# Kernel optimization log

Hardware: AMD Instinct MI355X
Metric: run time of the kernel (lower is better)

Reference implementation:

```python
import jax, jax.numpy as jnp
import numpy as np

DIM = 128
B, N = 2, 72


def setup_inputs() -> dict:
    key = jax.random.key(0)
    ks = jax.random.split(key, 6)
    s = 1.0 / np.sqrt(DIM)
    s3 = 1.0 / np.sqrt(3 * DIM)
    return {
        "node_emb": jax.random.normal(ks[0], (B * N, DIM), dtype=jnp.float32),
        "path_emb": jax.random.normal(ks[1], (B, N, N, DIM), dtype=jnp.float32),
        "W_hz": jax.random.uniform(ks[2], (DIM, DIM), minval=-s, maxval=s, dtype=jnp.float32),
        "b_hz": jax.random.uniform(ks[3], (DIM,), minval=-s, maxval=s, dtype=jnp.float32),
        "W_zz": jax.random.uniform(ks[4], (3 * DIM, DIM), minval=-s3, maxval=s3, dtype=jnp.float32),
        "b_zz": jax.random.uniform(ks[5], (DIM,), minval=-s3, maxval=s3, dtype=jnp.float32),
    }


def reference(node_emb, path_emb, W_hz, b_hz, W_zz, b_zz):
    b, n, _, d = path_emb.shape
    # z = W_hz(path_emb)
    z = jnp.einsum('bijd,de->bije', path_emb, W_hz) + b_hz
    # tropical (max-plus) triangle aggregation: out[b,i,j,d] = max_k z[b,i,k,d] + z[b,k,j,d]
    z_conv = jnp.max(z[:, :, :, None, :] + z[:, None, :, :, :], axis=2)  # (b,n,n,d)
    # path_aggr with mode 'max' -> elementwise max of z_conv and z
    z = jnp.maximum(z_conv, z)
    ne = node_emb.reshape(b, n, d)
    n_i = jnp.broadcast_to(ne[:, :, None, :], (b, n, n, d))
    n_j = jnp.broadcast_to(ne[:, None, :, :], (b, n, n, d))
    zc = jnp.concatenate([n_i, z, n_j], axis=-1)  # (b,n,n,3d)
    out = jax.nn.relu(jnp.einsum('bijc,ce->bije', zc, W_zz) + b_zz)
    return out
```

## Files before the change

kernel.cpp:

```cpp
#include <hip/hip_runtime.h>

#define DIM 128
#define NN 72
#define BB 2
#define NSQ (NN*NN)
#define NROWS (BB*NSQ)
#define BN (BB*NN)
#define ZBLOCKS (NROWS/16)
#define NODEBLK 9

__global__ __launch_bounds__(256, 4) void k_phase1(const float* __restrict__ path,
                                                   const float* __restrict__ Whz,
                                                   const float* __restrict__ bhz,
                                                   float* __restrict__ z,
                                                   float* __restrict__ zT,
                                                   const float* __restrict__ node,
                                                   const float* __restrict__ Wzz,
                                                   float* __restrict__ P1,
                                                   float* __restrict__ P3) {
    __shared__ float rows[16 * DIM];
    const int t = threadIdx.x;

    if (blockIdx.x >= NODEBLK) {
        const int r0 = (blockIdx.x - NODEBLK) * 16;
        {
            float4* rs = (float4*)rows;
            const float4* pg = (const float4*)(path + r0 * DIM);
            rs[t]       = pg[t];
            rs[t + 256] = pg[t + 256];
        }
        __syncthreads();

        const int e2 = t & 63;
        const int rg = t >> 6;
        float2 bz = *(const float2*)&bhz[2 * e2];
        float2 acc[4];
#pragma unroll
        for (int r = 0; r < 4; r++) acc[r] = bz;

        const float* Wp = Whz + 2 * e2;
        float2 w0[4], w1[4], n0[4], n1[4];
#pragma unroll
        for (int dd = 0; dd < 4; dd++) {
            w0[dd] = *(const float2*)&Wp[dd * DIM];
            w1[dd] = *(const float2*)&Wp[(4 + dd) * DIM];
        }
        for (int d8 = 0; d8 < 16; d8++) {
            if (d8 < 15) {
#pragma unroll
                for (int dd = 0; dd < 4; dd++) {
                    n0[dd] = *(const float2*)&Wp[(8 * d8 + 8 + dd) * DIM];
                    n1[dd] = *(const float2*)&Wp[(8 * d8 + 12 + dd) * DIM];
                }
            }
            float4 pa[4], pb[4];
#pragma unroll
            for (int r = 0; r < 4; r++) {
                pa[r] = *(const float4*)&rows[(rg + 4 * r) * DIM + 8 * d8];
                pb[r] = *(const float4*)&rows[(rg + 4 * r) * DIM + 8 * d8 + 4];
            }
#pragma unroll
            for (int dd = 0; dd < 4; dd++)
#pragma unroll
                for (int r = 0; r < 4; r++) {
                    float pv = ((const float*)&pa[r])[dd];
                    acc[r].x = fmaf(pv, w0[dd].x, acc[r].x);
                    acc[r].y = fmaf(pv, w0[dd].y, acc[r].y);
                }
#pragma unroll
            for (int dd = 0; dd < 4; dd++)
#pragma unroll
                for (int r = 0; r < 4; r++) {
                    float pv = ((const float*)&pb[r])[dd];
                    acc[r].x = fmaf(pv, w1[dd].x, acc[r].x);
                    acc[r].y = fmaf(pv, w1[dd].y, acc[r].y);
                }
#pragma unroll
            for (int dd = 0; dd < 4; dd++) { w0[dd] = n0[dd]; w1[dd] = n1[dd]; }
        }
#pragma unroll
        for (int r = 0; r < 4; r++) {
            int row = r0 + rg + 4 * r;
            *(float2*)&z[row * DIM + 2 * e2] = acc[r];
            int b  = row / NSQ;
            int ij = row - b * NSQ;
            int i  = ij / NN;
            int j  = ij - i * NN;
            *(float2*)&zT[(b * NSQ + j * NN + i) * DIM + 2 * e2] = acc[r];
        }
    } else {
        const int r0 = blockIdx.x * 16;
        {
            float4* rs = (float4*)rows;
            const float4* ng = (const float4*)(node + r0 * DIM);
            rs[t]       = ng[t];
            rs[t + 256] = ng[t + 256];
        }
        __syncthreads();

        const int e2 = t & 63;
        const int rg = t >> 6;
        float2 a1[4], a3[4];
#pragma unroll
        for (int r = 0; r < 4; r++) {
            a1[r] = make_float2(0.f, 0.f);
            a3[r] = make_float2(0.f, 0.f);
        }

        const float* W1p = Wzz + 2 * e2;
        const float* W3p = Wzz + 2 * DIM * DIM + 2 * e2;
        float2 u0[4], u1[4], v0[4], v1[4];
        float2 un0[4], un1[4], vn0[4], vn1[4];
#pragma unroll
        for (int dd = 0; dd < 4; dd++) {
            u0[dd] = *(const float2*)&W1p[dd * DIM];
            u1[dd] = *(const float2*)&W1p[(4 + dd) * DIM];
            v0[dd] = *(const float2*)&W3p[dd * DIM];
            v1[dd] = *(const float2*)&W3p[(4 + dd) * DIM];
        }
        for (int d8 = 0; d8 < 16; d8++) {
            if (d8 < 15) {
#pragma unroll
                for (int dd = 0; dd < 4; dd++) {
                    un0[dd] = *(const float2*)&W1p[(8 * d8 + 8 + dd) * DIM];
                    un1[dd] = *(const float2*)&W1p[(8 * d8 + 12 + dd) * DIM];
                    vn0[dd] = *(const float2*)&W3p[(8 * d8 + 8 + dd) * DIM];
                    vn1[dd] = *(const float2*)&W3p[(8 * d8 + 12 + dd) * DIM];
                }
            }
            float4 pa[4], pb[4];
#pragma unroll
            for (int r = 0; r < 4; r++) {
                pa[r] = *(const float4*)&rows[(rg + 4 * r) * DIM + 8 * d8];
                pb[r] = *(const float4*)&rows[(rg + 4 * r) * DIM + 8 * d8 + 4];
            }
#pragma unroll
            for (int dd = 0; dd < 4; dd++)
#pragma unroll
                for (int r = 0; r < 4; r++) {
                    float pv = ((const float*)&pa[r])[dd];
                    a1[r].x = fmaf(pv, u0[dd].x, a1[r].x);
                    a1[r].y = fmaf(pv, u0[dd].y, a1[r].y);
                    a3[r].x = fmaf(pv, v0[dd].x, a3[r].x);
                    a3[r].y = fmaf(pv, v0[dd].y, a3[r].y);
                }
#pragma unroll
            for (int dd = 0; dd < 4; dd++)
#pragma unroll
                for (int r = 0; r < 4; r++) {
                    float pv = ((const float*)&pb[r])[dd];
                    a1[r].x = fmaf(pv, u1[dd].x, a1[r].x);
                    a1[r].y = fmaf(pv, u1[dd].y, a1[r].y);
                    a3[r].x = fmaf(pv, v1[dd].x, a3[r].x);
                    a3[r].y = fmaf(pv, v1[dd].y, a3[r].y);
                }
#pragma unroll
            for (int dd = 0; dd < 4; dd++) {
                u0[dd] = un0[dd]; u1[dd] = un1[dd];
                v0[dd] = vn0[dd]; v1[dd] = vn1[dd];
            }
        }
#pragma unroll
        for (int r = 0; r < 4; r++) {
            int m = r0 + rg + 4 * r;
            *(float2*)&P1[m * DIM + 2 * e2] = a1[r];
            *(float2*)&P3[m * DIM + 2 * e2] = a3[r];
        }
    }
}

__global__ __launch_bounds__(256, 3) void k_trop_out(
        const float* __restrict__ z,   const float* __restrict__ zT,
        const float* __restrict__ Wzz, const float* __restrict__ bzz,
        const float* __restrict__ P1,  const float* __restrict__ P3,
        float* __restrict__ out) {
    __shared__ float rows[16 * DIM];
    __shared__ float comb[16 * DIM];
    const int t   = threadIdx.x;
    const int blk = blockIdx.x;
    const int b   = blk / 324;
    const int rem = blk - b * 324;
    const int it  = rem / 18;
    const int jt  = rem - it * 18;
    const int i0 = it * 4, j0 = jt * 4;
    const int d  = t & 127;
    const int ty = t >> 7;
    const float* zb  = z  + b * NSQ * DIM;
    const float* zTb = zT + b * NSQ * DIM;

    {
        float acc[16];
#pragma unroll
        for (int q = 0; q < 16; q++) acc[q] = -3.402823466e38f;

        float cur[32], nxt[32];
#pragma unroll
        for (int kk = 0; kk < 4; kk++) {
            int k = ty + 2 * kk;
#pragma unroll
            for (int s = 0; s < 4; s++) {
                cur[kk * 8 + s]     = zb [((i0 + s) * NN + k) * DIM + d];
                cur[kk * 8 + 4 + s] = zTb[((j0 + s) * NN + k) * DIM + d];
            }
        }
        for (int g = 0; g < 9; g++) {
            if (g < 8) {
#pragma unroll
                for (int kk = 0; kk < 4; kk++) {
                    int k = ty + 2 * kk + 8 * (g + 1);
#pragma unroll
                    for (int s = 0; s < 4; s++) {
                        nxt[kk * 8 + s]     = zb [((i0 + s) * NN + k) * DIM + d];
                        nxt[kk * 8 + 4 + s] = zTb[((j0 + s) * NN + k) * DIM + d];
                    }
                }
            }
#pragma unroll
            for (int kk = 0; kk < 4; kk++)
#pragma unroll
                for (int a = 0; a < 4; a++)
#pragma unroll
                    for (int c = 0; c < 4; c++)
                        acc[a * 4 + c] = fmaxf(acc[a * 4 + c],
                                               cur[kk * 8 + a] + cur[kk * 8 + 4 + c]);
#pragma unroll
            for (int q = 0; q < 32; q++) cur[q] = nxt[q];
        }

        if (ty == 1) {
#pragma unroll
            for (int q = 0; q < 16; q++) comb[q * DIM + d] = acc[q];
        }
        __syncthreads();
        if (ty == 0) {
#pragma unroll
            for (int a = 0; a < 4; a++)
#pragma unroll
                for (int c = 0; c < 4; c++) {
                    int q = a * 4 + c;
                    float m = fmaxf(acc[q], comb[q * DIM + d]);
                    int idx = ((i0 + a) * NN + (j0 + c)) * DIM + d;
                    rows[q * DIM + d] = fmaxf(m, zb[idx]);
                }
        }
    }
    __syncthreads();

    {
        const int e2 = t & 63;
        const int rg = t >> 6;
        float2 acc[4];
#pragma unroll
        for (int r = 0; r < 4; r++) acc[r] = make_float2(0.f, 0.f);

        const float* Wp = Wzz + DIM * DIM + 2 * e2;
        float2 w0[4], w1[4], n0[4], n1[4];
#pragma unroll
        for (int dd = 0; dd < 4; dd++) {
            w0[dd] = *(const float2*)&Wp[dd * DIM];
            w1[dd] = *(const float2*)&Wp[(4 + dd) * DIM];
        }
        for (int d8 = 0; d8 < 16; d8++) {
            if (d8 < 15) {
#pragma unroll
                for (int dd = 0; dd < 4; dd++) {
                    n0[dd] = *(const float2*)&Wp[(8 * d8 + 8 + dd) * DIM];
                    n1[dd] = *(const float2*)&Wp[(8 * d8 + 12 + dd) * DIM];
                }
            }
            float4 pa[4], pb[4];
#pragma unroll
            for (int r = 0; r < 4; r++) {
                pa[r] = *(const float4*)&rows[(rg + 4 * r) * DIM + 8 * d8];
                pb[r] = *(const float4*)&rows[(rg + 4 * r) * DIM + 8 * d8 + 4];
            }
#pragma unroll
            for (int dd = 0; dd < 4; dd++)
#pragma unroll
                for (int r = 0; r < 4; r++) {
                    float pv = ((const float*)&pa[r])[dd];
                    acc[r].x = fmaf(pv, w0[dd].x, acc[r].x);
                    acc[r].y = fmaf(pv, w0[dd].y, acc[r].y);
                }
#pragma unroll
            for (int dd = 0; dd < 4; dd++)
#pragma unroll
                for (int r = 0; r < 4; r++) {
                    float pv = ((const float*)&pb[r])[dd];
                    acc[r].x = fmaf(pv, w1[dd].x, acc[r].x);
                    acc[r].y = fmaf(pv, w1[dd].y, acc[r].y);
                }
#pragma unroll
            for (int dd = 0; dd < 4; dd++) { w0[dd] = n0[dd]; w1[dd] = n1[dd]; }
        }

        float2 bz = *(const float2*)&bzz[2 * e2];
#pragma unroll
        for (int r = 0; r < 4; r++) {
            int q = rg + 4 * r;
            int a = q >> 2, c = q & 3;
            int orow = b * NSQ + (i0 + a) * NN + (j0 + c);
            float2 v1 = *(const float2*)&P1[(b * NN + i0 + a) * DIM + 2 * e2];
            float2 v3 = *(const float2*)&P3[(b * NN + j0 + c) * DIM + 2 * e2];
            float ox = fmaxf(acc[r].x + v1.x + v3.x + bz.x, 0.f);
            float oy = fmaxf(acc[r].y + v1.y + v3.y + bz.y, 0.f);
            *(float2*)&out[orow * DIM + 2 * e2] = make_float2(ox, oy);
        }
    }
}

extern "C" void kernel_launch(void* const* d_in, const int* in_sizes, int n_in,
                              void* d_out, int out_size, void* d_ws, size_t ws_size,
                              hipStream_t stream) {
    const float* node = (const float*)d_in[0];
    const float* path = (const float*)d_in[1];
    const float* Whz  = (const float*)d_in[2];
    const float* bhz  = (const float*)d_in[3];
    const float* Wzz  = (const float*)d_in[4];
    const float* bzz  = (const float*)d_in[5];
    float* out = (float*)d_out;

    float* z  = (float*)d_ws;
    float* zT = z  + NROWS * DIM;
    float* P1 = zT + NROWS * DIM;
    float* P3 = P1 + BN * DIM;

    hipLaunchKernelGGL(k_phase1,   dim3(ZBLOCKS + NODEBLK), dim3(256), 0, stream,
                       path, Whz, bhz, z, zT, node, Wzz, P1, P3);
    hipLaunchKernelGGL(k_trop_out, dim3(BB * 18 * 18),      dim3(256), 0, stream,
                       z, zT, Wzz, bzz, P1, P3, out);
}
```

Baseline: 110.3 us.

## Halve tropical output tile to 2x4 and double-buffer k-loads without copies

The tropical max-plus kernel now processes a 2x4 (i,j) tile per block instead of 4x4, which doubles the grid to 1296 blocks and halves shared memory and register use so that occupancy can rise to 4 blocks per CU. The software pipeline now ping-pongs between two register buffers instead of copying nxt into cur each step. The output GEMV is restructured so each thread computes one output column for 4 rows with scalar loads. The smaller tile lowers register pressure and improves load balance, but each z column is reused across fewer outputs, so global traffic for z goes up, and the W rows are reloaded by twice as many blocks.

```diff
diff --git a/kernel.cpp b/kernel.cpp
--- a/kernel.cpp
+++ b/kernel.cpp
@@ -169,72 +169,72 @@
     }
 }
 
-__global__ __launch_bounds__(256, 3) void k_trop_out(
+__global__ __launch_bounds__(256, 4) void k_trop_out(
         const float* __restrict__ z,   const float* __restrict__ zT,
         const float* __restrict__ Wzz, const float* __restrict__ bzz,
         const float* __restrict__ P1,  const float* __restrict__ P3,
         float* __restrict__ out) {
-    __shared__ float rows[16 * DIM];
-    __shared__ float comb[16 * DIM];
+    __shared__ float rows[8 * DIM];
+    __shared__ float comb[8 * DIM];
     const int t   = threadIdx.x;
     const int blk = blockIdx.x;
-    const int b   = blk / 324;
-    const int rem = blk - b * 324;
+    const int b   = blk / 648;
+    const int rem = blk - b * 648;
     const int it  = rem / 18;
     const int jt  = rem - it * 18;
-    const int i0 = it * 4, j0 = jt * 4;
+    const int i0 = it * 2, j0 = jt * 4;
     const int d  = t & 127;
     const int ty = t >> 7;
     const float* zb  = z  + b * NSQ * DIM;
     const float* zTb = zT + b * NSQ * DIM;
 
     {
-        float acc[16];
-#pragma unroll
-        for (int q = 0; q < 16; q++) acc[q] = -3.402823466e38f;
-
-        float cur[32], nxt[32];
-#pragma unroll
-        for (int kk = 0; kk < 4; kk++) {
-            int k = ty + 2 * kk;
-#pragma unroll
-            for (int s = 0; s < 4; s++) {
-                cur[kk * 8 + s]     = zb [((i0 + s) * NN + k) * DIM + d];
-                cur[kk * 8 + 4 + s] = zTb[((j0 + s) * NN + k) * DIM + d];
-            }
-        }
-        for (int g = 0; g < 9; g++) {
-            if (g < 8) {
-#pragma unroll
-                for (int kk = 0; kk < 4; kk++) {
-                    int k = ty + 2 * kk + 8 * (g + 1);
-#pragma unroll
-                    for (int s = 0; s < 4; s++) {
-                        nxt[kk * 8 + s]     = zb [((i0 + s) * NN + k) * DIM + d];
-                        nxt[kk * 8 + 4 + s] = zTb[((j0 + s) * NN + k) * DIM + d];
-                    }
-                }
-            }
+        float acc[8];
+#pragma unroll
+        for (int q = 0; q < 8; q++) acc[q] = -3.402823466e38f;
+
+        float A[24], B[24];
+
+        auto loadg = [&](float* buf, int g) {
+#pragma unroll
+            for (int kk = 0; kk < 4; kk++) {
+                int k = ty + 2 * kk + 8 * g;
+#pragma unroll
+                for (int s = 0; s < 2; s++)
+                    buf[kk * 6 + s] = zb[((i0 + s) * NN + k) * DIM + d];
+#pragma unroll
+                for (int s = 0; s < 4; s++)
+                    buf[kk * 6 + 2 + s] = zTb[((j0 + s) * NN + k) * DIM + d];
+            }
+        };
+        auto compg = [&](const float* buf) {
 #pragma unroll
             for (int kk = 0; kk < 4; kk++)
 #pragma unroll
-                for (int a = 0; a < 4; a++)
+                for (int a = 0; a < 2; a++)
 #pragma unroll
                     for (int c = 0; c < 4; c++)
                         acc[a * 4 + c] = fmaxf(acc[a * 4 + c],
-                                               cur[kk * 8 + a] + cur[kk * 8 + 4 + c]);
-#pragma unroll
-            for (int q = 0; q < 32; q++) cur[q] = nxt[q];
-        }
+                                               buf[kk * 6 + a] + buf[kk * 6 + 2 + c]);
+        };
+
+        loadg(A, 0);
+        for (int g = 0; g < 8; g += 2) {
+            loadg(B, g + 1);
+            compg(A);
+            loadg(A, g + 2);
+            compg(B);
+        }
+        compg(A);
 
         if (ty == 1) {
 #pragma unroll
-            for (int q = 0; q < 16; q++) comb[q * DIM + d] = acc[q];
+            for (int q = 0; q < 8; q++) comb[q * DIM + d] = acc[q];
         }
         __syncthreads();
         if (ty == 0) {
 #pragma unroll
-            for (int a = 0; a < 4; a++)
+            for (int a = 0; a < 2; a++)
 #pragma unroll
                 for (int c = 0; c < 4; c++) {
                     int q = a * 4 + c;
@@ -247,64 +247,38 @@
     __syncthreads();
 
     {
-        const int e2 = t & 63;
-        const int rg = t >> 6;
-        float2 acc[4];
-#pragma unroll
-        for (int r = 0; r < 4; r++) acc[r] = make_float2(0.f, 0.f);
-
-        const float* Wp = Wzz + DIM * DIM + 2 * e2;
-        float2 w0[4], w1[4], n0[4], n1[4];
-#pragma unroll
-        for (int dd = 0; dd < 4; dd++) {
-            w0[dd] = *(const float2*)&Wp[dd * DIM];
-            w1[dd] = *(const float2*)&Wp[(4 + dd) * DIM];
-        }
+        const int e  = t & 127;
+        const int rr = t >> 7;
+        float a4[4] = {0.f, 0.f, 0.f, 0.f};
+
+        const float* Wp = Wzz + DIM * DIM + e;
+        float w[8], wn[8];
+#pragma unroll
+        for (int dd = 0; dd < 8; dd++) w[dd] = Wp[dd * DIM];
         for (int d8 = 0; d8 < 16; d8++) {
             if (d8 < 15) {
 #pragma unroll
-                for (int dd = 0; dd < 4; dd++) {
-                    n0[dd] = *(const float2*)&Wp[(8 * d8 + 8 + dd) * DIM];
-                    n1[dd] = *(const float2*)&Wp[(8 * d8 + 12 + dd) * DIM];
-                }
-            }
-            float4 pa[4], pb[4];
-#pragma unroll
-            for (int r = 0; r < 4; r++) {
-                pa[r] = *(const float4*)&rows[(rg + 4 * r) * DIM + 8 * d8];
-                pb[r] = *(const float4*)&rows[(rg + 4 * r) * DIM + 8 * d8 + 4];
-            }
-#pragma unroll
-            for (int dd = 0; dd < 4; dd++)
-#pragma unroll
-                for (int r = 0; r < 4; r++) {
-                    float pv = ((const float*)&pa[r])[dd];
-                    acc[r].x = fmaf(pv, w0[dd].x, acc[r].x);
-                    acc[r].y = fmaf(pv, w0[dd].y, acc[r].y);
-                }
-#pragma unroll
-            for (int dd = 0; dd < 4; dd++)
-#pragma unroll
-                for (int r = 0; r < 4; r++) {
-                    float pv = ((const float*)&pb[r])[dd];
-                    acc[r].x = fmaf(pv, w1[dd].x, acc[r].x);
-                    acc[r].y = fmaf(pv, w1[dd].y, acc[r].y);
-                }
-#pragma unroll
-            for (int dd = 0; dd < 4; dd++) { w0[dd] = n0[dd]; w1[dd] = n1[dd]; }
-        }
-
-        float2 bz = *(const float2*)&bzz[2 * e2];
-#pragma unroll
-        for (int r = 0; r < 4; r++) {
-            int q = rg + 4 * r;
+                for (int dd = 0; dd < 8; dd++)
+                    wn[dd] = Wp[(8 * d8 + 8 + dd) * DIM];
+            }
+#pragma unroll
+            for (int dd = 0; dd < 8; dd++)
+#pragma unroll
+                for (int s = 0; s < 4; s++)
+                    a4[s] = fmaf(rows[(rr * 4 + s) * DIM + 8 * d8 + dd], w[dd], a4[s]);
+#pragma unroll
+            for (int dd = 0; dd < 8; dd++) w[dd] = wn[dd];
+        }
+
+        float bz = bzz[e];
+#pragma unroll
+        for (int s = 0; s < 4; s++) {
+            int q = rr * 4 + s;
             int a = q >> 2, c = q & 3;
             int orow = b * NSQ + (i0 + a) * NN + (j0 + c);
-            float2 v1 = *(const float2*)&P1[(b * NN + i0 + a) * DIM + 2 * e2];
-            float2 v3 = *(const float2*)&P3[(b * NN + j0 + c) * DIM + 2 * e2];
-            float ox = fmaxf(acc[r].x + v1.x + v3.x + bz.x, 0.f);
-            float oy = fmaxf(acc[r].y + v1.y + v3.y + bz.y, 0.f);
-            *(float2*)&out[orow * DIM + 2 * e2] = make_float2(ox, oy);
+            float v1 = P1[(b * NN + i0 + a) * DIM + e];
+            float v3 = P3[(b * NN + j0 + c) * DIM + e];
+            out[orow * DIM + e] = fmaxf(a4[s] + v1 + v3 + bz, 0.f);
         }
     }
 }
@@ -327,6 +301,6 @@
 
     hipLaunchKernelGGL(k_phase1,   dim3(ZBLOCKS + NODEBLK), dim3(256), 0, stream,
                        path, Whz, bhz, z, zT, node, Wzz, P1, P3);
-    hipLaunchKernelGGL(k_trop_out, dim3(BB * 18 * 18),      dim3(256), 0, stream,
+    hipLaunchKernelGGL(k_trop_out, dim3(BB * 36 * 18),      dim3(256), 0, stream,
                        z, zT, Wzz, bzz, P1, P3, out);
 }
```

Measured after the change: 108.4 us. No clear change (-1.7%).

## Fuse both phases into one persistent kernel with a software grid barrier

Applied to the files above, without the earlier changes.

Merges the projection/node-precompute kernel and the tropical-aggregation/output kernel into one 648-block launch, separated by an atomic-counter grid barrier. The first nine blocks also compute the node projections after their z rows. This removes a kernel launch and the inter-kernel drain gap, but adds a memset, a spin barrier that relies on all 648 blocks being co-resident (launch bounds 3 per SIMD), and extra work on nine blocks.

```diff
diff --git a/kernel.cpp b/kernel.cpp
--- a/kernel.cpp
+++ b/kernel.cpp
@@ -6,23 +6,36 @@
 #define NSQ (NN*NN)
 #define NROWS (BB*NSQ)
 #define BN (BB*NN)
-#define ZBLOCKS (NROWS/16)
-#define NODEBLK 9
-
-__global__ __launch_bounds__(256, 4) void k_phase1(const float* __restrict__ path,
-                                                   const float* __restrict__ Whz,
-                                                   const float* __restrict__ bhz,
-                                                   float* __restrict__ z,
-                                                   float* __restrict__ zT,
-                                                   const float* __restrict__ node,
-                                                   const float* __restrict__ Wzz,
-                                                   float* __restrict__ P1,
-                                                   float* __restrict__ P3) {
+#define GRID 648
+
+__device__ __forceinline__ void grid_barrier(unsigned* cnt) {
+    __syncthreads();
+    if (threadIdx.x == 0) {
+        __threadfence();
+        atomicAdd(cnt, 1u);
+        while (__hip_atomic_load(cnt, __ATOMIC_RELAXED,
+                                 __HIP_MEMORY_SCOPE_AGENT) < (unsigned)GRID) {
+            __builtin_amdgcn_s_sleep(8);
+        }
+    }
+    __syncthreads();
+    __threadfence();
+}
+
+__global__ __launch_bounds__(256, 3) void k_fused(
+        const float* __restrict__ path, const float* __restrict__ Whz,
+        const float* __restrict__ bhz,  const float* __restrict__ node,
+        const float* __restrict__ Wzz,  const float* __restrict__ bzz,
+        float* __restrict__ z,  float* __restrict__ zT,
+        float* __restrict__ P1, float* __restrict__ P3,
+        unsigned* cnt, float* __restrict__ out) {
     __shared__ float rows[16 * DIM];
-    const int t = threadIdx.x;
-
-    if (blockIdx.x >= NODEBLK) {
-        const int r0 = (blockIdx.x - NODEBLK) * 16;
+    __shared__ float comb[16 * DIM];
+    const int t   = threadIdx.x;
+    const int blk = blockIdx.x;
+
+    {
+        const int r0 = blk * 16;
         {
             float4* rs = (float4*)rows;
             const float4* pg = (const float4*)(path + r0 * DIM);
@@ -88,8 +101,11 @@
             int j  = ij - i * NN;
             *(float2*)&zT[(b * NSQ + j * NN + i) * DIM + 2 * e2] = acc[r];
         }
-    } else {
-        const int r0 = blockIdx.x * 16;
+    }
+
+    if (blk < 9) {
+        __syncthreads();
+        const int r0 = blk * 16;
         {
             float4* rs = (float4*)rows;
             const float4* ng = (const float4*)(node + r0 * DIM);
@@ -106,7 +122,6 @@
             a1[r] = make_float2(0.f, 0.f);
             a3[r] = make_float2(0.f, 0.f);
         }
-
         const float* W1p = Wzz + 2 * e2;
         const float* W3p = Wzz + 2 * DIM * DIM + 2 * e2;
         float2 u0[4], u1[4], v0[4], v1[4];
@@ -167,17 +182,9 @@
             *(float2*)&P3[m * DIM + 2 * e2] = a3[r];
         }
     }
-}
-
-__global__ __launch_bounds__(256, 3) void k_trop_out(
-        const float* __restrict__ z,   const float* __restrict__ zT,
-        const float* __restrict__ Wzz, const float* __restrict__ bzz,
-        const float* __restrict__ P1,  const float* __restrict__ P3,
-        float* __restrict__ out) {
-    __shared__ float rows[16 * DIM];
-    __shared__ float comb[16 * DIM];
-    const int t   = threadIdx.x;
-    const int blk = blockIdx.x;
+
+    grid_barrier(cnt);
+
     const int b   = blk / 324;
     const int rem = blk - b * 324;
     const int it  = rem / 18;
@@ -187,7 +194,6 @@
     const int ty = t >> 7;
     const float* zb  = z  + b * NSQ * DIM;
     const float* zTb = zT + b * NSQ * DIM;
-
     {
         float acc[16];
 #pragma unroll
@@ -320,13 +326,14 @@
     const float* bzz  = (const float*)d_in[5];
     float* out = (float*)d_out;
 
-    float* z  = (float*)d_ws;
+    unsigned* cnt = (unsigned*)d_ws;
+    float* base = (float*)d_ws;
+    float* z  = base + 256;
     float* zT = z  + NROWS * DIM;
     float* P1 = zT + NROWS * DIM;
     float* P3 = P1 + BN * DIM;
 
-    hipLaunchKernelGGL(k_phase1,   dim3(ZBLOCKS + NODEBLK), dim3(256), 0, stream,
-                       path, Whz, bhz, z, zT, node, Wzz, P1, P3);
-    hipLaunchKernelGGL(k_trop_out, dim3(BB * 18 * 18),      dim3(256), 0, stream,
-                       z, zT, Wzz, bzz, P1, P3, out);
+    hipMemsetAsync(d_ws, 0, 64, stream);
+    hipLaunchKernelGGL(k_fused, dim3(GRID), dim3(256), 0, stream,
+                       path, Whz, bhz, node, Wzz, bzz, z, zT, P1, P3, cnt, out);
 }
```

New measurement: 218.9 us. 98.5% more time.
